# Kernel optimization log

Measured on AMD Instinct MI355X. Metric: run time of the kernel, lower is better.

The kernel has to match this reference:

```python
import jax, jax.numpy as jnp
import numpy as np

B, N, C_Z, C_H = 1, 512, 128, 128
EPS = 1e-5


def _layer_norm(x, w, b):
    mu = jnp.mean(x, axis=-1, keepdims=True)
    var = jnp.mean(jnp.square(x - mu), axis=-1, keepdims=True)
    return (x - mu) * jax.lax.rsqrt(var + EPS) * w + b


def setup_inputs() -> dict:
    key = jax.random.key(0)
    ks = jax.random.split(key, 8)

    def lin(k, out_d, in_d, scale=0.02):
        kw, kb = jax.random.split(k)
        return (jax.random.normal(kw, (out_d, in_d), jnp.float32) * scale,
                jax.random.normal(kb, (out_d,), jnp.float32) * scale)

    inp = {}
    inp["z"] = jax.random.normal(ks[0], (B, N, N, C_Z), jnp.float32)
    inp["mask"] = jnp.ones((B, N, N), jnp.float32)
    inp["ln_in_w"] = jnp.ones((C_Z,), jnp.float32)
    inp["ln_in_b"] = jnp.zeros((C_Z,), jnp.float32)
    inp["ag_w"], inp["ag_b"] = lin(ks[1], C_H, C_Z)
    inp["ap_w"], inp["ap_b"] = lin(ks[2], C_H, C_Z)
    inp["bg_w"], inp["bg_b"] = lin(ks[3], C_H, C_Z)
    inp["bp_w"], inp["bp_b"] = lin(ks[4], C_H, C_Z)
    inp["ln_out_w"] = jnp.ones((C_H,), jnp.float32)
    inp["ln_out_b"] = jnp.zeros((C_H,), jnp.float32)
    inp["z_w"], inp["z_b"] = lin(ks[5], C_Z, C_H)
    inp["g_w"], inp["g_b"] = lin(ks[6], C_Z, C_Z)
    return inp


def reference(z, mask, ln_in_w, ln_in_b, ag_w, ag_b, ap_w, ap_b,
              bg_w, bg_b, bp_w, bp_b, ln_out_w, ln_out_b, z_w, z_b, g_w, g_b):
    # z: [B, N, N, C_z], mask: [B, N, N]
    m = mask[..., None]
    zn = _layer_norm(z, ln_in_w, ln_in_b)
    # gated projections, masked
    a = m * jax.nn.sigmoid(zn @ ag_w.T + ag_b) * (zn @ ap_w.T + ap_b)
    b = m * jax.nn.sigmoid(zn @ bg_w.T + bg_b) * (zn @ bp_w.T + bp_b)
    # outgoing triangle update: out[b,i,j,d] = sum_k a[b,i,k,d] * b[b,k,j,d]
    x = jnp.einsum('bikd,bkjd->bijd', a, b)
    x = _layer_norm(x, ln_out_w, ln_out_b)
    x = x @ z_w.T + z_b
    g = jax.nn.sigmoid(zn @ g_w.T + g_b)
    return x * g
```

## Files before the change

kernel.cpp:

```cpp
#include <hip/hip_runtime.h>
#include <hip/hip_bf16.h>


typedef __attribute__((ext_vector_type(8))) short  bfrag;
typedef __attribute__((ext_vector_type(4))) float  f4acc;

static __device__ __forceinline__ unsigned short f2bf(float f) {
    union { float f; unsigned u; } v; v.f = f;
    unsigned r = v.u + 0x7FFFu + ((v.u >> 16) & 1u);
    return (unsigned short)(r >> 16);
}
static __device__ __forceinline__ float bf2f(unsigned short h) {
    union { unsigned u; float f; } v; v.u = ((unsigned)h) << 16;
    return v.f;
}
static __device__ __forceinline__ float sigmoidf_(float x) {
    return 1.0f / (1.0f + __expf(-x));
}

__global__ __launch_bounds__(256) void k0_pack(
    const float* __restrict__ w0, const float* __restrict__ w1,
    const float* __restrict__ w2, const float* __restrict__ w3,
    const float* __restrict__ w4, const float* __restrict__ w5,
    unsigned short* __restrict__ Wbf)
{
    int idx = blockIdx.x * 256 + threadIdx.x;
    int m = idx >> 14, r = idx & 16383;
    const float* src = (m == 0) ? w0 : (m == 1) ? w1 : (m == 2) ? w2
                     : (m == 3) ? w3 : (m == 4) ? w4 : w5;
    Wbf[idx] = f2bf(src[r]);
}

__global__ __launch_bounds__(256) void k1_ln(
    const float* __restrict__ z, const float* __restrict__ lnw,
    const float* __restrict__ lnb, unsigned short* __restrict__ zn_t)
{
    __shared__ unsigned short zn[64 * 136];

    const int t = threadIdx.x;
    const int p0 = blockIdx.x << 6;

    {
        int pos = t >> 2, sub = t & 3;
        const float4* zp = (const float4*)z + (size_t)(p0 + pos) * 32 + sub * 8;
        float4 v[8];
        float s = 0.0f, sq = 0.0f;
#pragma unroll
        for (int i = 0; i < 8; ++i) {
            v[i] = zp[i];
            s  += v[i].x + v[i].y + v[i].z + v[i].w;
            sq += v[i].x*v[i].x + v[i].y*v[i].y + v[i].z*v[i].z + v[i].w*v[i].w;
        }
        s += __shfl_xor(s, 1); sq += __shfl_xor(sq, 1);
        s += __shfl_xor(s, 2); sq += __shfl_xor(sq, 2);
        float mean = s * 0.0078125f;
        float var  = sq * 0.0078125f - mean * mean;
        float rstd = rsqrtf(var + 1e-5f);
#pragma unroll
        for (int i = 0; i < 8; ++i) {
            int ch = sub * 32 + i * 4;
            float4 wv = *(const float4*)(lnw + ch);
            float4 bv = *(const float4*)(lnb + ch);
            unsigned short h0 = f2bf((v[i].x - mean) * rstd * wv.x + bv.x);
            unsigned short h1 = f2bf((v[i].y - mean) * rstd * wv.y + bv.y);
            unsigned short h2 = f2bf((v[i].z - mean) * rstd * wv.z + bv.z);
            unsigned short h3 = f2bf((v[i].w - mean) * rstd * wv.w + bv.w);
            uint2 pk;
            pk.x = (unsigned)h0 | ((unsigned)h1 << 16);
            pk.y = (unsigned)h2 | ((unsigned)h3 << 16);
            *(uint2*)&zn[pos * 136 + ch] = pk;
        }
    }
    __syncthreads();

#pragma unroll
    for (int it = 0; it < 4; ++it) {
        int e = it * 256 + t;
        float4 vv = *(const float4*)&zn[(e >> 4) * 136 + (e & 15) * 8];
        *(float4*)(zn_t + (size_t)p0 * 128 + (size_t)e * 8) = vv;
    }
}

template <int NMAT, bool HAS_G>
static __device__ __forceinline__ void proj_phase(
    const unsigned short* zn, unsigned short (*stg)[16 * 72],
    const float* mask_s,
    const unsigned short* __restrict__ Wbf,
    const float* __restrict__ bias0, const float* __restrict__ bias1,
    const float* __restrict__ bias2,
    unsigned short* __restrict__ out_ab, size_t ab_base,
    unsigned short* __restrict__ out_g, size_t g_base, int t)
{
    const int w = t >> 6, l = t & 63, col = l & 15, q = l >> 4;
    const int dl = l >> 3, seg = l & 7;

    for (int dt = w; dt < 8; dt += 4) {
        f4acc acc[4][NMAT];
#pragma unroll
        for (int mt = 0; mt < 4; ++mt)
#pragma unroll
            for (int m = 0; m < NMAT; ++m)
#pragma unroll
                for (int r = 0; r < 4; ++r) acc[mt][m][r] = 0.0f;

#pragma unroll
        for (int ks = 0; ks < 4; ++ks) {
            bfrag bf[NMAT];
#pragma unroll
            for (int m = 0; m < NMAT; ++m)
                bf[m] = *(const bfrag*)(Wbf + ((m * 128 + dt * 16 + col) * 128
                                               + ks * 32 + q * 8));
#pragma unroll
            for (int mt = 0; mt < 4; ++mt) {
                bfrag af = *(const bfrag*)&zn[(mt * 16 + col) * 136 + ks * 32 + q * 8];
#pragma unroll
                for (int m = 0; m < NMAT; ++m)
                    acc[mt][m] = __builtin_amdgcn_mfma_f32_16x16x32_bf16(
                        af, bf[m], acc[mt][m], 0, 0, 0);
            }
        }

        int d = dt * 16 + col;
        float ba = bias0[d], bb = bias1[d];
        float bg = HAS_G ? bias2[d] : 0.0f;
        unsigned short pg[4][4];

#pragma unroll
        for (int mt = 0; mt < 4; ++mt) {
            unsigned short pa[4];
#pragma unroll
            for (int r = 0; r < 4; ++r) {
                int pos = mt * 16 + q * 4 + r;
                float gate = sigmoidf_(acc[mt][0][r] + ba);
                pa[r] = f2bf(mask_s[pos] * gate * (acc[mt][1][r] + bb));
                if (HAS_G) pg[mt][r] = f2bf(sigmoidf_(acc[mt][NMAT - 1][r] + bg));
            }
            *(uint2*)&stg[w][col * 72 + mt * 16 + q * 4] = *(const uint2*)pa;
        }
#pragma unroll
        for (int it = 0; it < 2; ++it) {
            int dd = it * 8 + dl;
            float4 va = *(const float4*)&stg[w][dd * 72 + seg * 8];
            *(float4*)(out_ab + (size_t)(dt * 16 + dd) * 262144 + ab_base + seg * 8) = va;
        }

        if (HAS_G) {
#pragma unroll
            for (int mt = 0; mt < 4; ++mt)
                *(uint2*)&stg[w][col * 72 + mt * 16 + q * 4] = *(const uint2*)pg[mt];
#pragma unroll
            for (int it = 0; it < 2; ++it) {
                int dd = it * 8 + dl;
                float4 vg = *(const float4*)&stg[w][dd * 72 + seg * 8];
                *(float4*)(out_g + (size_t)(dt * 16 + dd) * 262144 + g_base + seg * 8) = vg;
            }
        }
    }
}

__global__ __launch_bounds__(256) void k1p_kern(
    const unsigned short* __restrict__ zn_t, const float* __restrict__ mask,
    const unsigned short* __restrict__ Wbf,
    const float* __restrict__ ag_b, const float* __restrict__ ap_b,
    const float* __restrict__ g_b,
    unsigned short* __restrict__ a_t, unsigned short* __restrict__ g_t)
{
    __shared__ unsigned short zn[64 * 136];
    __shared__ unsigned short stg[4][16 * 72];
    __shared__ float mask_s[64];

    const int t = threadIdx.x;
    const int p0 = blockIdx.x << 6;

    if (t < 64) mask_s[t] = mask[p0 + t];

#pragma unroll
    for (int it = 0; it < 4; ++it) {
        int e = it * 256 + t;
        *(float4*)&zn[(e >> 4) * 136 + (e & 15) * 8] =
            *(const float4*)(zn_t + (size_t)p0 * 128 + (size_t)e * 8);
    }
    __syncthreads();

    proj_phase<3, true>(zn, stg, mask_s, Wbf, ag_b, ap_b, g_b,
                        a_t, (size_t)p0, g_t, (size_t)p0, t);
}

__global__ __launch_bounds__(256) void k1b_kern(
    const unsigned short* __restrict__ zn_t, const float* __restrict__ mask,
    const unsigned short* __restrict__ Wbf,
    const float* __restrict__ bg_b, const float* __restrict__ bp_b,
    unsigned short* __restrict__ b_tt)
{
    __shared__ unsigned short zn[64 * 136];
    __shared__ unsigned short stg[4][16 * 72];
    __shared__ float mask_s[64];

    const int t = threadIdx.x;
    const int c  = blockIdx.x & 511;
    const int r0 = (blockIdx.x >> 9) << 6;

    if (t < 64) mask_s[t] = mask[(r0 + t) * 512 + c];

#pragma unroll
    for (int it = 0; it < 4; ++it) {
        int e = it * 256 + t;
        int pl = e >> 4, chunk = e & 15;
        float4 vv = *(const float4*)(zn_t + ((size_t)(r0 + pl) * 512 + c) * 128
                                     + chunk * 8);
        *(float4*)&zn[pl * 136 + chunk * 8] = vv;
    }
    __syncthreads();

    proj_phase<2, false>(zn, stg, mask_s, Wbf, bg_b, bp_b, nullptr,
                         b_tt, (size_t)c * 512 + r0, nullptr, 0, t);
}

__global__ __launch_bounds__(256) void k2_gemm(
    const unsigned short* __restrict__ a_t,
    const unsigned short* __restrict__ b_tt,
    unsigned short* __restrict__ x_t)
{
    __shared__ unsigned short As[128 * 40];
    __shared__ unsigned short Bs[128 * 40];

    const int t = threadIdx.x;
    int bx   = blockIdx.x;
    int d4ti = (bx & 7) + ((bx >> 5) << 3);
    int tj   = (bx >> 3) & 3;
    int d    = d4ti >> 2, ti = d4ti & 3;
    int i0 = ti * 128, j0 = tj * 128;
    size_t abase = (size_t)d * 262144 + (size_t)i0 * 512;
    size_t bbase = (size_t)d * 262144 + (size_t)j0 * 512;

    const int w = t >> 6, l = t & 63, col = l & 15, q = l >> 4;
    const int wi = w >> 1, wj = w & 1;

    f4acc acc[4][4];
#pragma unroll
    for (int mt = 0; mt < 4; ++mt)
#pragma unroll
        for (int nt = 0; nt < 4; ++nt)
#pragma unroll
            for (int r = 0; r < 4; ++r) acc[mt][nt][r] = 0.0f;

    for (int k0 = 0; k0 < 512; k0 += 32) {
#pragma unroll
        for (int rep = 0; rep < 2; ++rep) {
            int e = rep * 256 + t;
            int row = e >> 2, ch = e & 3;
            *(float4*)&As[row * 40 + ch * 8] =
                *(const float4*)(a_t + abase + (size_t)row * 512 + k0 + ch * 8);
            *(float4*)&Bs[row * 40 + ch * 8] =
                *(const float4*)(b_tt + bbase + (size_t)row * 512 + k0 + ch * 8);
        }
        __syncthreads();

        bfrag af[4], bf[4];
#pragma unroll
        for (int mt = 0; mt < 4; ++mt)
            af[mt] = *(const bfrag*)&As[(wi * 64 + mt * 16 + col) * 40 + q * 8];
#pragma unroll
        for (int nt = 0; nt < 4; ++nt)
            bf[nt] = *(const bfrag*)&Bs[(wj * 64 + nt * 16 + col) * 40 + q * 8];
#pragma unroll
        for (int mt = 0; mt < 4; ++mt)
#pragma unroll
            for (int nt = 0; nt < 4; ++nt)
                acc[mt][nt] = __builtin_amdgcn_mfma_f32_16x16x32_bf16(
                    af[mt], bf[nt], acc[mt][nt], 0, 0, 0);
        __syncthreads();
    }

    size_t obase = (size_t)d * 262144;
#pragma unroll
    for (int mt = 0; mt < 4; ++mt)
#pragma unroll
        for (int nt = 0; nt < 4; ++nt)
#pragma unroll
            for (int r = 0; r < 4; ++r) {
                int i_l = wi * 64 + mt * 16 + q * 4 + r;
                int j_l = wj * 64 + nt * 16 + col;
                x_t[obase + (size_t)(i0 + i_l) * 512 + j0 + j_l] = f2bf(acc[mt][nt][r]);
            }
}

__global__ __launch_bounds__(256) void k3_out(
    const unsigned short* __restrict__ x_t,
    const unsigned short* __restrict__ g_t,
    const unsigned short* __restrict__ Wz,
    const float* __restrict__ z_b,
    const float* __restrict__ lnow, const float* __restrict__ lnob,
    float* __restrict__ out)
{
    __shared__ unsigned short xs[128 * 72];
    __shared__ unsigned short gs[128 * 72];
    __shared__ unsigned short xn[64 * 136];
    __shared__ float low_s[128], lob_s[128];

    const int t = threadIdx.x;
    const int p0 = blockIdx.x << 6;

    if (t < 128) { low_s[t] = lnow[t]; lob_s[t] = lnob[t]; }
#pragma unroll
    for (int rep = 0; rep < 4; ++rep) {
        int e = rep * 256 + t;
        int dd = e >> 3, ch = e & 7;
        *(float4*)&xs[dd * 72 + ch * 8] =
            *(const float4*)(x_t + (size_t)dd * 262144 + p0 + ch * 8);
        *(float4*)&gs[dd * 72 + ch * 8] =
            *(const float4*)(g_t + (size_t)dd * 262144 + p0 + ch * 8);
    }
    __syncthreads();

    {
        int pos = t >> 2, sub = t & 3;
        float vals[32];
        float s = 0.0f, sq = 0.0f;
#pragma unroll
        for (int i = 0; i < 32; ++i) {
            float v = bf2f(xs[(sub * 32 + i) * 72 + pos]);
            vals[i] = v; s += v; sq += v * v;
        }
        s += __shfl_xor(s, 1); sq += __shfl_xor(sq, 1);
        s += __shfl_xor(s, 2); sq += __shfl_xor(sq, 2);
        float mean = s * 0.0078125f;
        float var  = sq * 0.0078125f - mean * mean;
        float rstd = rsqrtf(var + 1e-5f);
#pragma unroll
        for (int i = 0; i < 32; ++i) {
            int dd = sub * 32 + i;
            xn[pos * 136 + dd] = f2bf((vals[i] - mean) * rstd * low_s[dd] + lob_s[dd]);
        }
    }
    __syncthreads();

    const int w = t >> 6, l = t & 63, col = l & 15, q = l >> 4;
    f4acc acc[4][2];
#pragma unroll
    for (int mt = 0; mt < 4; ++mt)
#pragma unroll
        for (int i = 0; i < 2; ++i)
#pragma unroll
            for (int r = 0; r < 4; ++r) acc[mt][i][r] = 0.0f;

#pragma unroll
    for (int ks = 0; ks < 4; ++ks) {
        bfrag b0 = *(const bfrag*)(Wz + ((w * 16 + col) * 128 + ks * 32 + q * 8));
        bfrag b1 = *(const bfrag*)(Wz + (((w + 4) * 16 + col) * 128 + ks * 32 + q * 8));
#pragma unroll
        for (int mt = 0; mt < 4; ++mt) {
            bfrag af = *(const bfrag*)&xn[(mt * 16 + col) * 136 + ks * 32 + q * 8];
            acc[mt][0] = __builtin_amdgcn_mfma_f32_16x16x32_bf16(af, b0, acc[mt][0], 0, 0, 0);
            acc[mt][1] = __builtin_amdgcn_mfma_f32_16x16x32_bf16(af, b1, acc[mt][1], 0, 0, 0);
        }
    }

#pragma unroll
    for (int i = 0; i < 2; ++i) {
        int n = (w + i * 4) * 16 + col;
        float zb = z_b[n];
#pragma unroll
        for (int mt = 0; mt < 4; ++mt)
#pragma unroll
            for (int r = 0; r < 4; ++r) {
                int pos = mt * 16 + q * 4 + r;
                float gv = bf2f(gs[n * 72 + pos]);
                out[(size_t)(p0 + pos) * 128 + n] = (acc[mt][i][r] + zb) * gv;
            }
    }
}

extern "C" void kernel_launch(void* const* d_in, const int* in_sizes, int n_in,
                              void* d_out, int out_size, void* d_ws, size_t ws_size,
                              hipStream_t stream)
{
    const float* z    = (const float*)d_in[0];
    const float* mask = (const float*)d_in[1];
    const float* lnw  = (const float*)d_in[2];
    const float* lnb  = (const float*)d_in[3];
    const float* ag_w = (const float*)d_in[4];
    const float* ag_b = (const float*)d_in[5];
    const float* ap_w = (const float*)d_in[6];
    const float* ap_b = (const float*)d_in[7];
    const float* bg_w = (const float*)d_in[8];
    const float* bg_b = (const float*)d_in[9];
    const float* bp_w = (const float*)d_in[10];
    const float* bp_b = (const float*)d_in[11];
    const float* lnow = (const float*)d_in[12];
    const float* lnob = (const float*)d_in[13];
    const float* z_w  = (const float*)d_in[14];
    const float* z_b  = (const float*)d_in[15];
    const float* g_w  = (const float*)d_in[16];
    const float* g_b  = (const float*)d_in[17];
    float* out = (float*)d_out;

    char* ws = (char*)d_ws;
    unsigned short* Wbf  = (unsigned short*)ws;
    unsigned short* a_t  = (unsigned short*)(ws + 196608);
    unsigned short* b_tt = a_t  + 33554432;
    unsigned short* g_t  = b_tt + 33554432;
    unsigned short* x_t  = g_t  + 33554432;
    unsigned short* zn_t = x_t;

    k0_pack<<<384, 256, 0, stream>>>(ag_w, ap_w, g_w, bg_w, bp_w, z_w, Wbf);
    k1_ln<<<4096, 256, 0, stream>>>(z, lnw, lnb, zn_t);
    k1p_kern<<<4096, 256, 0, stream>>>(zn_t, mask, Wbf,
                                       ag_b, ap_b, g_b, a_t, g_t);
    k1b_kern<<<4096, 256, 0, stream>>>(zn_t, mask, Wbf + 3 * 16384,
                                       bg_b, bp_b, b_tt);
    k2_gemm<<<2048, 256, 0, stream>>>(a_t, b_tt, x_t);
    k3_out<<<4096, 256, 0, stream>>>(x_t, g_t, Wbf + 5 * 16384, z_b, lnow, lnob, out);

    (void)in_sizes; (void)n_in; (void)out_size; (void)ws_size;
}
```

Measured before the change: 543.2 us.

## Recompute output gate in final kernel from normalized input instead of storing it

The gate projection sigmoid(zn·Wg+b) is no longer computed in the first projection kernel and written out as a bf16 tensor. The final output kernel now reloads the normalized input tile and does the gate GEMM alongside the output projection, applying the sigmoid in the epilogue. This removes one full-size intermediate write and read, trading them for a zn_t reread and extra MFMA work in the last kernel. zn_t now gets its own workspace buffer instead of aliasing x_t, and the LDS buffer for x is reused for the normalized tile, with an added barrier.

```diff
diff --git a/kernel.cpp b/kernel.cpp
--- a/kernel.cpp
+++ b/kernel.cpp
@@ -81,40 +81,37 @@
     }
 }
 
-template <int NMAT, bool HAS_G>
-static __device__ __forceinline__ void proj_phase(
+static __device__ __forceinline__ void proj_phase2(
     const unsigned short* zn, unsigned short (*stg)[16 * 72],
     const float* mask_s,
     const unsigned short* __restrict__ Wbf,
     const float* __restrict__ bias0, const float* __restrict__ bias1,
-    const float* __restrict__ bias2,
-    unsigned short* __restrict__ out_ab, size_t ab_base,
-    unsigned short* __restrict__ out_g, size_t g_base, int t)
+    unsigned short* __restrict__ out_ab, size_t ab_base, int t)
 {
     const int w = t >> 6, l = t & 63, col = l & 15, q = l >> 4;
     const int dl = l >> 3, seg = l & 7;
 
     for (int dt = w; dt < 8; dt += 4) {
-        f4acc acc[4][NMAT];
+        f4acc acc[4][2];
 #pragma unroll
         for (int mt = 0; mt < 4; ++mt)
 #pragma unroll
-            for (int m = 0; m < NMAT; ++m)
+            for (int m = 0; m < 2; ++m)
 #pragma unroll
                 for (int r = 0; r < 4; ++r) acc[mt][m][r] = 0.0f;
 
 #pragma unroll
         for (int ks = 0; ks < 4; ++ks) {
-            bfrag bf[NMAT];
-#pragma unroll
-            for (int m = 0; m < NMAT; ++m)
+            bfrag bf[2];
+#pragma unroll
+            for (int m = 0; m < 2; ++m)
                 bf[m] = *(const bfrag*)(Wbf + ((m * 128 + dt * 16 + col) * 128
                                                + ks * 32 + q * 8));
 #pragma unroll
             for (int mt = 0; mt < 4; ++mt) {
                 bfrag af = *(const bfrag*)&zn[(mt * 16 + col) * 136 + ks * 32 + q * 8];
 #pragma unroll
-                for (int m = 0; m < NMAT; ++m)
+                for (int m = 0; m < 2; ++m)
                     acc[mt][m] = __builtin_amdgcn_mfma_f32_16x16x32_bf16(
                         af, bf[m], acc[mt][m], 0, 0, 0);
             }
@@ -122,8 +119,6 @@
 
         int d = dt * 16 + col;
         float ba = bias0[d], bb = bias1[d];
-        float bg = HAS_G ? bias2[d] : 0.0f;
-        unsigned short pg[4][4];
 
 #pragma unroll
         for (int mt = 0; mt < 4; ++mt) {
@@ -133,7 +128,6 @@
                 int pos = mt * 16 + q * 4 + r;
                 float gate = sigmoidf_(acc[mt][0][r] + ba);
                 pa[r] = f2bf(mask_s[pos] * gate * (acc[mt][1][r] + bb));
-                if (HAS_G) pg[mt][r] = f2bf(sigmoidf_(acc[mt][NMAT - 1][r] + bg));
             }
             *(uint2*)&stg[w][col * 72 + mt * 16 + q * 4] = *(const uint2*)pa;
         }
@@ -143,18 +137,6 @@
             float4 va = *(const float4*)&stg[w][dd * 72 + seg * 8];
             *(float4*)(out_ab + (size_t)(dt * 16 + dd) * 262144 + ab_base + seg * 8) = va;
         }
-
-        if (HAS_G) {
-#pragma unroll
-            for (int mt = 0; mt < 4; ++mt)
-                *(uint2*)&stg[w][col * 72 + mt * 16 + q * 4] = *(const uint2*)pg[mt];
-#pragma unroll
-            for (int it = 0; it < 2; ++it) {
-                int dd = it * 8 + dl;
-                float4 vg = *(const float4*)&stg[w][dd * 72 + seg * 8];
-                *(float4*)(out_g + (size_t)(dt * 16 + dd) * 262144 + g_base + seg * 8) = vg;
-            }
-        }
     }
 }
 
@@ -162,8 +144,7 @@
     const unsigned short* __restrict__ zn_t, const float* __restrict__ mask,
     const unsigned short* __restrict__ Wbf,
     const float* __restrict__ ag_b, const float* __restrict__ ap_b,
-    const float* __restrict__ g_b,
-    unsigned short* __restrict__ a_t, unsigned short* __restrict__ g_t)
+    unsigned short* __restrict__ a_t)
 {
     __shared__ unsigned short zn[64 * 136];
     __shared__ unsigned short stg[4][16 * 72];
@@ -182,8 +163,7 @@
     }
     __syncthreads();
 
-    proj_phase<3, true>(zn, stg, mask_s, Wbf, ag_b, ap_b, g_b,
-                        a_t, (size_t)p0, g_t, (size_t)p0, t);
+    proj_phase2(zn, stg, mask_s, Wbf, ag_b, ap_b, a_t, (size_t)p0, t);
 }
 
 __global__ __launch_bounds__(256) void k1b_kern(
@@ -212,8 +192,7 @@
     }
     __syncthreads();
 
-    proj_phase<2, false>(zn, stg, mask_s, Wbf, bg_b, bp_b, nullptr,
-                         b_tt, (size_t)c * 512 + r0, nullptr, 0, t);
+    proj_phase2(zn, stg, mask_s, Wbf, bg_b, bp_b, b_tt, (size_t)c * 512 + r0, t);
 }
 
 __global__ __launch_bounds__(256) void k2_gemm(
@@ -287,15 +266,15 @@
 
 __global__ __launch_bounds__(256) void k3_out(
     const unsigned short* __restrict__ x_t,
-    const unsigned short* __restrict__ g_t,
+    const unsigned short* __restrict__ zn_t,
     const unsigned short* __restrict__ Wz,
-    const float* __restrict__ z_b,
+    const unsigned short* __restrict__ Wg,
+    const float* __restrict__ z_b, const float* __restrict__ g_b,
     const float* __restrict__ lnow, const float* __restrict__ lnob,
     float* __restrict__ out)
 {
     __shared__ unsigned short xs[128 * 72];
-    __shared__ unsigned short gs[128 * 72];
-    __shared__ unsigned short xn[64 * 136];
+    __shared__ unsigned short zs[64 * 136];
     __shared__ float low_s[128], lob_s[128];
 
     const int t = threadIdx.x;
@@ -308,8 +287,12 @@
         int dd = e >> 3, ch = e & 7;
         *(float4*)&xs[dd * 72 + ch * 8] =
             *(const float4*)(x_t + (size_t)dd * 262144 + p0 + ch * 8);
-        *(float4*)&gs[dd * 72 + ch * 8] =
-            *(const float4*)(g_t + (size_t)dd * 262144 + p0 + ch * 8);
+    }
+#pragma unroll
+    for (int it = 0; it < 4; ++it) {
+        int e = it * 256 + t;
+        *(float4*)&zs[(e >> 4) * 136 + (e & 15) * 8] =
+            *(const float4*)(zn_t + (size_t)p0 * 128 + (size_t)e * 8);
     }
     __syncthreads();
 
@@ -327,45 +310,51 @@
         float mean = s * 0.0078125f;
         float var  = sq * 0.0078125f - mean * mean;
         float rstd = rsqrtf(var + 1e-5f);
+        __syncthreads();
 #pragma unroll
         for (int i = 0; i < 32; ++i) {
             int dd = sub * 32 + i;
-            xn[pos * 136 + dd] = f2bf((vals[i] - mean) * rstd * low_s[dd] + lob_s[dd]);
+            xs[pos * 136 + dd] = f2bf((vals[i] - mean) * rstd * low_s[dd] + lob_s[dd]);
         }
     }
     __syncthreads();
 
     const int w = t >> 6, l = t & 63, col = l & 15, q = l >> 4;
-    f4acc acc[4][2];
+    f4acc acc[4][2], accg[4][2];
 #pragma unroll
     for (int mt = 0; mt < 4; ++mt)
 #pragma unroll
         for (int i = 0; i < 2; ++i)
 #pragma unroll
-            for (int r = 0; r < 4; ++r) acc[mt][i][r] = 0.0f;
+            for (int r = 0; r < 4; ++r) { acc[mt][i][r] = 0.0f; accg[mt][i][r] = 0.0f; }
 
 #pragma unroll
     for (int ks = 0; ks < 4; ++ks) {
         bfrag b0 = *(const bfrag*)(Wz + ((w * 16 + col) * 128 + ks * 32 + q * 8));
         bfrag b1 = *(const bfrag*)(Wz + (((w + 4) * 16 + col) * 128 + ks * 32 + q * 8));
+        bfrag g0 = *(const bfrag*)(Wg + ((w * 16 + col) * 128 + ks * 32 + q * 8));
+        bfrag g1 = *(const bfrag*)(Wg + (((w + 4) * 16 + col) * 128 + ks * 32 + q * 8));
 #pragma unroll
         for (int mt = 0; mt < 4; ++mt) {
-            bfrag af = *(const bfrag*)&xn[(mt * 16 + col) * 136 + ks * 32 + q * 8];
-            acc[mt][0] = __builtin_amdgcn_mfma_f32_16x16x32_bf16(af, b0, acc[mt][0], 0, 0, 0);
-            acc[mt][1] = __builtin_amdgcn_mfma_f32_16x16x32_bf16(af, b1, acc[mt][1], 0, 0, 0);
+            bfrag ax = *(const bfrag*)&xs[(mt * 16 + col) * 136 + ks * 32 + q * 8];
+            bfrag az = *(const bfrag*)&zs[(mt * 16 + col) * 136 + ks * 32 + q * 8];
+            acc[mt][0]  = __builtin_amdgcn_mfma_f32_16x16x32_bf16(ax, b0, acc[mt][0], 0, 0, 0);
+            acc[mt][1]  = __builtin_amdgcn_mfma_f32_16x16x32_bf16(ax, b1, acc[mt][1], 0, 0, 0);
+            accg[mt][0] = __builtin_amdgcn_mfma_f32_16x16x32_bf16(az, g0, accg[mt][0], 0, 0, 0);
+            accg[mt][1] = __builtin_amdgcn_mfma_f32_16x16x32_bf16(az, g1, accg[mt][1], 0, 0, 0);
         }
     }
 
 #pragma unroll
     for (int i = 0; i < 2; ++i) {
         int n = (w + i * 4) * 16 + col;
-        float zb = z_b[n];
+        float zb = z_b[n], gb = g_b[n];
 #pragma unroll
         for (int mt = 0; mt < 4; ++mt)
 #pragma unroll
             for (int r = 0; r < 4; ++r) {
                 int pos = mt * 16 + q * 4 + r;
-                float gv = bf2f(gs[n * 72 + pos]);
+                float gv = sigmoidf_(accg[mt][i][r] + gb);
                 out[(size_t)(p0 + pos) * 128 + n] = (acc[mt][i][r] + zb) * gv;
             }
     }
@@ -399,18 +388,18 @@
     unsigned short* Wbf  = (unsigned short*)ws;
     unsigned short* a_t  = (unsigned short*)(ws + 196608);
     unsigned short* b_tt = a_t  + 33554432;
-    unsigned short* g_t  = b_tt + 33554432;
-    unsigned short* x_t  = g_t  + 33554432;
-    unsigned short* zn_t = x_t;
+    unsigned short* x_t  = b_tt + 33554432;
+    unsigned short* zn_t = x_t  + 33554432;
 
     k0_pack<<<384, 256, 0, stream>>>(ag_w, ap_w, g_w, bg_w, bp_w, z_w, Wbf);
     k1_ln<<<4096, 256, 0, stream>>>(z, lnw, lnb, zn_t);
     k1p_kern<<<4096, 256, 0, stream>>>(zn_t, mask, Wbf,
-                                       ag_b, ap_b, g_b, a_t, g_t);
+                                       ag_b, ap_b, a_t);
     k1b_kern<<<4096, 256, 0, stream>>>(zn_t, mask, Wbf + 3 * 16384,
                                        bg_b, bp_b, b_tt);
     k2_gemm<<<2048, 256, 0, stream>>>(a_t, b_tt, x_t);
-    k3_out<<<4096, 256, 0, stream>>>(x_t, g_t, Wbf + 5 * 16384, z_b, lnow, lnob, out);
+    k3_out<<<4096, 256, 0, stream>>>(x_t, zn_t, Wbf + 5 * 16384, Wbf + 2 * 16384,
+                                     z_b, g_b, lnow, lnob, out);
 
     (void)in_sizes; (void)n_in; (void)out_size; (void)ws_size;
 }
```

Measured after the change: 508.5 us. 6.4% less time.
